# Kernel optimization log

Measured on AMD Instinct MI355X. Metric: run time of the kernel, lower is better.

Reference implementation:

```python
import jax, jax.numpy as jnp
import numpy as np

N_SRC = 20000
N_TAR = 20000
DIM = 3


def setup_inputs() -> dict:
    key = jax.random.key(0)
    k1, k2 = jax.random.split(key)
    src_V = jax.random.normal(k1, (N_SRC, DIM), dtype=jnp.float32)
    tar_V = jax.random.normal(k2, (N_TAR, DIM), dtype=jnp.float32)
    return {"src_V": src_V, "tar_V": tar_V}


def reference(src_V, tar_V):
    # Brute-force 1-NN replacing the CPU cKDTree query.
    # Squared distances: ||t||^2 - 2 t.s^T + ||s||^2  -> [M, N]
    d2 = (
        jnp.sum(tar_V * tar_V, axis=1, keepdims=True)
        - 2.0 * (tar_V @ src_V.T)
        + jnp.sum(src_V * src_V, axis=1)[None, :]
    )
    ii = jnp.argmin(d2, axis=1)          # nearest src index per tar point
    diff = src_V[ii] - tar_V             # gather + residual, [M, 3]
    return 0.5 * jnp.sum(diff * diff)
```

## Files before the change

### kernel.cpp

```cpp
#include <hip/hip_runtime.h>
#include <float.h>

#define N_SRC 20000
#define N_TAR 20000
#define TPB 512
#define SPLITS 16
#define TILES 40
#define TGRP 79
#define FBLOCKS ((N_TAR + 255) / 256)

typedef _Float16 half8 __attribute__((ext_vector_type(8)));
typedef float floatx16 __attribute__((ext_vector_type(16)));

__global__ __launch_bounds__(TPB) void nn_mfma(
    const float* __restrict__ src, const float* __restrict__ tar,
    float* __restrict__ part, float* __restrict__ out)
{
    if (blockIdx.x == 0 && blockIdx.y == 0 && threadIdx.x == 0) out[0] = 0.f;

    __shared__ alignas(16) _Float16 lds[TILES * 32 * 16];

    const int tid  = threadIdx.x;
    const int lane = tid & 63;
    const int col  = lane & 31;
    const int half = (lane >> 5) & 1;
    const int wave = tid >> 6;

    const int sbase = blockIdx.y * (TILES * 32);
    for (int ls = tid; ls < TILES * 32; ls += TPB) {
        const int s = sbase + ls;
        half8 f0 = {0, 0, 0, 0, 0, 0, 0, 0};
        half8 f1 = {0, 0, 0, 0, 0, 0, 0, 0};
        if (s < N_SRC) {
            const float x = src[s * 3 + 0];
            const float y = src[s * 3 + 1];
            const float z = src[s * 3 + 2];
            const _Float16 xh = (_Float16)x, yh = (_Float16)y, zh = (_Float16)z;
            const _Float16 xl = (_Float16)(x - (float)xh);
            const _Float16 yl = (_Float16)(y - (float)yh);
            const _Float16 zl = (_Float16)(z - (float)zh);
            const float nrm = 0.5f * (x * x + y * y + z * z);
            const _Float16 nh = (_Float16)nrm;
            const _Float16 nl = (_Float16)(nrm - (float)nh);
            f0 = (half8){xh, yh, zh, xh, yh, zh, xl, yl};
            f1 = (half8){zl, nh, nl, 0, 0, 0, 0, 0};
        } else {
            f1 = (half8){0, (_Float16)30000.f, 0, 0, 0, 0, 0, 0};
        }
        *(half8*)&lds[ls * 16 + 0] = f0;
        *(half8*)&lds[ls * 16 + 8] = f1;
    }

    const int strip = blockIdx.x * 8 + wave;
    const int t = min(strip * 32 + col, N_TAR - 1);
    const float tx = tar[t * 3 + 0];
    const float ty = tar[t * 3 + 1];
    const float tz = tar[t * 3 + 2];
    const _Float16 txh = (_Float16)tx, tyh = (_Float16)ty, tzh = (_Float16)tz;
    const _Float16 txl = (_Float16)(tx - (float)txh);
    const _Float16 tyl = (_Float16)(ty - (float)tyh);
    const _Float16 tzl = (_Float16)(tz - (float)tzh);
    half8 a;
    if (half == 0)
        a = (half8){-txh, -tyh, -tzh, -txl, -tyl, -tzl, -txh, -tyh};
    else
        a = (half8){-tzh, (_Float16)1.f, (_Float16)1.f, 0, 0, 0, 0, 0};

    __syncthreads();

    floatx16 m;
#pragma unroll
    for (int i = 0; i < 16; ++i) m[i] = FLT_MAX;
    const floatx16 zero = {};
    const int foff = col * 16 + half * 8;
#pragma unroll 2
    for (int tile = 0; tile < TILES; ++tile) {
        const half8 b = *(const half8*)&lds[tile * 512 + foff];
        const floatx16 d = __builtin_amdgcn_mfma_f32_32x32x16_f16(a, b, zero, 0, 0, 0);
#pragma unroll
        for (int i = 0; i < 16; ++i) m[i] = fminf(m[i], d[i]);
    }

#pragma unroll
    for (int i = 0; i < 16; ++i) {
        m[i] = fminf(m[i], __shfl_xor(m[i], 1));
        m[i] = fminf(m[i], __shfl_xor(m[i], 2));
        m[i] = fminf(m[i], __shfl_xor(m[i], 4));
        m[i] = fminf(m[i], __shfl_xor(m[i], 8));
        m[i] = fminf(m[i], __shfl_xor(m[i], 16));
    }
    if (col == 0) {
#pragma unroll
        for (int i = 0; i < 16; ++i) {
            const int row = (i & 3) + 8 * (i >> 2) + 4 * half;
            const int tt = min(strip * 32 + row, N_TAR - 1);
            part[blockIdx.y * N_TAR + tt] = m[i];
        }
    }
}

__global__ __launch_bounds__(256) void nn_finalize(
    const float* __restrict__ tar, const float* __restrict__ part,
    float* __restrict__ out)
{
    const int t = blockIdx.x * 256 + threadIdx.x;
    float contrib = 0.f;
    if (t < N_TAR) {
        float m = FLT_MAX;
#pragma unroll
        for (int c = 0; c < SPLITS; ++c) m = fminf(m, part[c * N_TAR + t]);
        const float tx = tar[t * 3 + 0];
        const float ty = tar[t * 3 + 1];
        const float tz = tar[t * 3 + 2];
        contrib = 0.5f * (tx * tx + ty * ty + tz * tz) + m;
    }
    for (int off = 32; off > 0; off >>= 1)
        contrib += __shfl_down(contrib, off);
    __shared__ float red[4];
    if ((threadIdx.x & 63) == 0) red[threadIdx.x >> 6] = contrib;
    __syncthreads();
    if (threadIdx.x == 0) {
        float s = 0.f;
#pragma unroll
        for (int w = 0; w < 4; ++w) s += red[w];
        atomicAdd(out, s);
    }
}

extern "C" void kernel_launch(void* const* d_in, const int* in_sizes, int n_in,
                              void* d_out, int out_size, void* d_ws, size_t ws_size,
                              hipStream_t stream) {
    const float* src = (const float*)d_in[0];
    const float* tar = (const float*)d_in[1];
    float* out = (float*)d_out;
    float* part = (float*)d_ws;

    dim3 grid1(TGRP, SPLITS);
    nn_mfma<<<grid1, TPB, 0, stream>>>(src, tar, part, out);
    nn_finalize<<<FBLOCKS, 256, 0, stream>>>(tar, part, out);
}
```

Baseline: 77.78 us.

## Process two target strips per wave to reuse LDS source tiles

Each wave now handles two 32-point target strips, and the grid is halved to 40 target groups. Every pair of source tiles loaded from LDS feeds four MFMAs instead of one per load, which cuts LDS traffic and the per-block staging of source points into LDS. In exchange the kernel uses more registers (two accumulators, two A operands) and launches half as many blocks, which lowers occupancy and parallelism.

```diff
diff --git a/kernel.cpp b/kernel.cpp
--- a/kernel.cpp
+++ b/kernel.cpp
@@ -6,7 +6,8 @@
 #define TPB 512
 #define SPLITS 16
 #define TILES 40
-#define TGRP 79
+#define TGRP 40
+#define NSTRIPS (TGRP * 8)
 #define FBLOCKS ((N_TAR + 255) / 256)
 
 typedef _Float16 half8 __attribute__((ext_vector_type(8)));
@@ -51,50 +52,81 @@
         *(half8*)&lds[ls * 16 + 8] = f1;
     }
 
-    const int strip = blockIdx.x * 8 + wave;
-    const int t = min(strip * 32 + col, N_TAR - 1);
-    const float tx = tar[t * 3 + 0];
-    const float ty = tar[t * 3 + 1];
-    const float tz = tar[t * 3 + 2];
-    const _Float16 txh = (_Float16)tx, tyh = (_Float16)ty, tzh = (_Float16)tz;
-    const _Float16 txl = (_Float16)(tx - (float)txh);
-    const _Float16 tyl = (_Float16)(ty - (float)tyh);
-    const _Float16 tzl = (_Float16)(tz - (float)tzh);
-    half8 a;
-    if (half == 0)
-        a = (half8){-txh, -tyh, -tzh, -txl, -tyl, -tzl, -txh, -tyh};
-    else
-        a = (half8){-tzh, (_Float16)1.f, (_Float16)1.f, 0, 0, 0, 0, 0};
+    const int strip0 = blockIdx.x * 8 + wave;
+    const int strip1 = strip0 + NSTRIPS;
+    half8 a0, a1;
+    {
+        const int t = min(strip0 * 32 + col, N_TAR - 1);
+        const float tx = tar[t * 3 + 0];
+        const float ty = tar[t * 3 + 1];
+        const float tz = tar[t * 3 + 2];
+        const _Float16 txh = (_Float16)tx, tyh = (_Float16)ty, tzh = (_Float16)tz;
+        const _Float16 txl = (_Float16)(tx - (float)txh);
+        const _Float16 tyl = (_Float16)(ty - (float)tyh);
+        const _Float16 tzl = (_Float16)(tz - (float)tzh);
+        if (half == 0)
+            a0 = (half8){-txh, -tyh, -tzh, -txl, -tyl, -tzl, -txh, -tyh};
+        else
+            a0 = (half8){-tzh, (_Float16)1.f, (_Float16)1.f, 0, 0, 0, 0, 0};
+    }
+    {
+        const int t = min(strip1 * 32 + col, N_TAR - 1);
+        const float tx = tar[t * 3 + 0];
+        const float ty = tar[t * 3 + 1];
+        const float tz = tar[t * 3 + 2];
+        const _Float16 txh = (_Float16)tx, tyh = (_Float16)ty, tzh = (_Float16)tz;
+        const _Float16 txl = (_Float16)(tx - (float)txh);
+        const _Float16 tyl = (_Float16)(ty - (float)tyh);
+        const _Float16 tzl = (_Float16)(tz - (float)tzh);
+        if (half == 0)
+            a1 = (half8){-txh, -tyh, -tzh, -txl, -tyl, -tzl, -txh, -tyh};
+        else
+            a1 = (half8){-tzh, (_Float16)1.f, (_Float16)1.f, 0, 0, 0, 0, 0};
+    }
 
     __syncthreads();
 
-    floatx16 m;
+    floatx16 m0, m1;
 #pragma unroll
-    for (int i = 0; i < 16; ++i) m[i] = FLT_MAX;
+    for (int i = 0; i < 16; ++i) { m0[i] = FLT_MAX; m1[i] = FLT_MAX; }
     const floatx16 zero = {};
     const int foff = col * 16 + half * 8;
-#pragma unroll 2
-    for (int tile = 0; tile < TILES; ++tile) {
-        const half8 b = *(const half8*)&lds[tile * 512 + foff];
-        const floatx16 d = __builtin_amdgcn_mfma_f32_32x32x16_f16(a, b, zero, 0, 0, 0);
+    for (int tp = 0; tp < TILES; tp += 2) {
+        const half8 b0 = *(const half8*)&lds[tp * 512 + foff];
+        const half8 b1 = *(const half8*)&lds[(tp + 1) * 512 + foff];
+        const floatx16 d0 = __builtin_amdgcn_mfma_f32_32x32x16_f16(a0, b0, zero, 0, 0, 0);
+        const floatx16 d1 = __builtin_amdgcn_mfma_f32_32x32x16_f16(a0, b1, zero, 0, 0, 0);
 #pragma unroll
-        for (int i = 0; i < 16; ++i) m[i] = fminf(m[i], d[i]);
+        for (int i = 0; i < 16; ++i)
+            m0[i] = fminf(fminf(d0[i], d1[i]), m0[i]);
+        const floatx16 d2 = __builtin_amdgcn_mfma_f32_32x32x16_f16(a1, b0, zero, 0, 0, 0);
+        const floatx16 d3 = __builtin_amdgcn_mfma_f32_32x32x16_f16(a1, b1, zero, 0, 0, 0);
+#pragma unroll
+        for (int i = 0; i < 16; ++i)
+            m1[i] = fminf(fminf(d2[i], d3[i]), m1[i]);
     }
 
 #pragma unroll
     for (int i = 0; i < 16; ++i) {
-        m[i] = fminf(m[i], __shfl_xor(m[i], 1));
-        m[i] = fminf(m[i], __shfl_xor(m[i], 2));
-        m[i] = fminf(m[i], __shfl_xor(m[i], 4));
-        m[i] = fminf(m[i], __shfl_xor(m[i], 8));
-        m[i] = fminf(m[i], __shfl_xor(m[i], 16));
+        m0[i] = fminf(m0[i], __shfl_xor(m0[i], 1));
+        m1[i] = fminf(m1[i], __shfl_xor(m1[i], 1));
+        m0[i] = fminf(m0[i], __shfl_xor(m0[i], 2));
+        m1[i] = fminf(m1[i], __shfl_xor(m1[i], 2));
+        m0[i] = fminf(m0[i], __shfl_xor(m0[i], 4));
+        m1[i] = fminf(m1[i], __shfl_xor(m1[i], 4));
+        m0[i] = fminf(m0[i], __shfl_xor(m0[i], 8));
+        m1[i] = fminf(m1[i], __shfl_xor(m1[i], 8));
+        m0[i] = fminf(m0[i], __shfl_xor(m0[i], 16));
+        m1[i] = fminf(m1[i], __shfl_xor(m1[i], 16));
     }
     if (col == 0) {
 #pragma unroll
         for (int i = 0; i < 16; ++i) {
             const int row = (i & 3) + 8 * (i >> 2) + 4 * half;
-            const int tt = min(strip * 32 + row, N_TAR - 1);
-            part[blockIdx.y * N_TAR + tt] = m[i];
+            const int t0 = min(strip0 * 32 + row, N_TAR - 1);
+            const int t1 = min(strip1 * 32 + row, N_TAR - 1);
+            part[blockIdx.y * N_TAR + t0] = m0[i];
+            part[blockIdx.y * N_TAR + t1] = m1[i];
         }
     }
 }
```

After: 80.81 us. +3.9%, slower.

## Fuse NN min and reduction into one kernel with atomic-max partials and last-block finalize

Applied to the files above, without the earlier changes.

Merges the two kernels into one. Each wave now processes three target strips against the same staged source tile, which reuses the LDS B operands across more MFMAs. The LDS layout is XOR-swizzled to reduce bank conflicts, and shuffles are replaced by DPP row rotations. Per-target minima are combined through order-preserving atomicMax on a global buffer, and the last block to finish does the final sum and resets the buffer. This removes one kernel launch and the partial-array traffic, at the cost of a global atomic counter, persistent device state, and heavy reliance on correct memory fences.

```diff
diff --git a/kernel.cpp b/kernel.cpp
--- a/kernel.cpp
+++ b/kernel.cpp
@@ -5,28 +5,37 @@
 #define N_TAR 20000
 #define TPB 512
 #define SPLITS 16
+#define COLS 32
+#define NBLOCKS (COLS * SPLITS)
 #define TILES 40
-#define TGRP 79
-#define FBLOCKS ((N_TAR + 255) / 256)
+#define SRC_PER_SPLIT 1250
+#define KSTRIPS 3
+#define NSTRIP 625
 
 typedef _Float16 half8 __attribute__((ext_vector_type(8)));
 typedef float floatx16 __attribute__((ext_vector_type(16)));
 
-__global__ __launch_bounds__(TPB) void nn_mfma(
+__device__ unsigned g_part[N_TAR];
+__device__ unsigned g_done = 0;
+
+#define ROTMIN(v, ctrl) \
+    fminf(v, __int_as_float(__builtin_amdgcn_mov_dpp(__float_as_int(v), ctrl, 0xF, 0xF, false)))
+
+__global__ __launch_bounds__(TPB, 4) void nn_fused(
     const float* __restrict__ src, const float* __restrict__ tar,
-    float* __restrict__ part, float* __restrict__ out)
+    float* __restrict__ out)
 {
-    if (blockIdx.x == 0 && blockIdx.y == 0 && threadIdx.x == 0) out[0] = 0.f;
-
-    __shared__ alignas(16) _Float16 lds[TILES * 32 * 16];
+    __shared__ alignas(16) _Float16 bstage[TILES * 512];
+    __shared__ bool is_last;
+    __shared__ float red[8];
 
     const int tid  = threadIdx.x;
     const int lane = tid & 63;
     const int col  = lane & 31;
-    const int half = (lane >> 5) & 1;
+    const int hsel = (lane >> 5) & 1;
     const int wave = tid >> 6;
 
-    const int sbase = blockIdx.y * (TILES * 32);
+    const int sbase = blockIdx.y * SRC_PER_SPLIT;
     for (int ls = tid; ls < TILES * 32; ls += TPB) {
         const int s = sbase + ls;
         half8 f0 = {0, 0, 0, 0, 0, 0, 0, 0};
@@ -47,83 +56,113 @@
         } else {
             f1 = (half8){0, (_Float16)30000.f, 0, 0, 0, 0, 0, 0};
         }
-        *(half8*)&lds[ls * 16 + 0] = f0;
-        *(half8*)&lds[ls * 16 + 8] = f1;
+        const int tile = ls >> 5, c = ls & 31;
+        const int n0 = c * 2, n1 = c * 2 + 1;
+        const int o0 = n0 ^ ((n0 >> 3) & 7);
+        const int o1 = n1 ^ ((n1 >> 3) & 7);
+        *(half8*)&bstage[tile * 512 + o0 * 8] = f0;
+        *(half8*)&bstage[tile * 512 + o1 * 8] = f1;
     }
 
-    const int strip = blockIdx.x * 8 + wave;
-    const int t = min(strip * 32 + col, N_TAR - 1);
-    const float tx = tar[t * 3 + 0];
-    const float ty = tar[t * 3 + 1];
-    const float tz = tar[t * 3 + 2];
-    const _Float16 txh = (_Float16)tx, tyh = (_Float16)ty, tzh = (_Float16)tz;
-    const _Float16 txl = (_Float16)(tx - (float)txh);
-    const _Float16 tyl = (_Float16)(ty - (float)tyh);
-    const _Float16 tzl = (_Float16)(tz - (float)tzh);
-    half8 a;
-    if (half == 0)
-        a = (half8){-txh, -tyh, -tzh, -txl, -tyl, -tzl, -txh, -tyh};
-    else
-        a = (half8){-tzh, (_Float16)1.f, (_Float16)1.f, 0, 0, 0, 0, 0};
+    const int strip0 = blockIdx.x * 8 + wave;
+    half8 a[KSTRIPS];
+    bool valid[KSTRIPS];
+#pragma unroll
+    for (int k = 0; k < KSTRIPS; ++k) {
+        const int sk = strip0 + k * 256;
+        valid[k] = (sk < NSTRIP);
+        const int t = min(sk * 32 + col, N_TAR - 1);
+        const float tx = tar[t * 3 + 0];
+        const float ty = tar[t * 3 + 1];
+        const float tz = tar[t * 3 + 2];
+        const _Float16 txh = (_Float16)tx, tyh = (_Float16)ty, tzh = (_Float16)tz;
+        const _Float16 txl = (_Float16)(tx - (float)txh);
+        const _Float16 tyl = (_Float16)(ty - (float)tyh);
+        const _Float16 tzl = (_Float16)(tz - (float)tzh);
+        if (hsel == 0)
+            a[k] = (half8){-txh, -tyh, -tzh, -txl, -tyl, -tzl, -txh, -tyh};
+        else
+            a[k] = (half8){-tzh, (_Float16)1.f, (_Float16)1.f, 0, 0, 0, 0, 0};
+    }
 
     __syncthreads();
 
-    floatx16 m;
+    floatx16 m0, m1, m2;
 #pragma unroll
-    for (int i = 0; i < 16; ++i) m[i] = FLT_MAX;
+    for (int i = 0; i < 16; ++i) { m0[i] = FLT_MAX; m1[i] = FLT_MAX; m2[i] = FLT_MAX; }
     const floatx16 zero = {};
-    const int foff = col * 16 + half * 8;
-#pragma unroll 2
-    for (int tile = 0; tile < TILES; ++tile) {
-        const half8 b = *(const half8*)&lds[tile * 512 + foff];
-        const floatx16 d = __builtin_amdgcn_mfma_f32_32x32x16_f16(a, b, zero, 0, 0, 0);
+    const int nrd = 2 * col + hsel;
+    const int foff = (nrd ^ ((nrd >> 3) & 7)) * 8;
+    for (int tp = 0; tp < TILES; tp += 2) {
+        const half8 b0 = *(const half8*)&bstage[tp * 512 + foff];
+        const half8 b1 = *(const half8*)&bstage[(tp + 1) * 512 + foff];
+        floatx16 d0, d1;
+        d0 = __builtin_amdgcn_mfma_f32_32x32x16_f16(a[0], b0, zero, 0, 0, 0);
+        d1 = __builtin_amdgcn_mfma_f32_32x32x16_f16(a[0], b1, zero, 0, 0, 0);
 #pragma unroll
-        for (int i = 0; i < 16; ++i) m[i] = fminf(m[i], d[i]);
+        for (int i = 0; i < 16; ++i) m0[i] = fminf(fminf(d0[i], d1[i]), m0[i]);
+        d0 = __builtin_amdgcn_mfma_f32_32x32x16_f16(a[1], b0, zero, 0, 0, 0);
+        d1 = __builtin_amdgcn_mfma_f32_32x32x16_f16(a[1], b1, zero, 0, 0, 0);
+#pragma unroll
+        for (int i = 0; i < 16; ++i) m1[i] = fminf(fminf(d0[i], d1[i]), m1[i]);
+        d0 = __builtin_amdgcn_mfma_f32_32x32x16_f16(a[2], b0, zero, 0, 0, 0);
+        d1 = __builtin_amdgcn_mfma_f32_32x32x16_f16(a[2], b1, zero, 0, 0, 0);
+#pragma unroll
+        for (int i = 0; i < 16; ++i) m2[i] = fminf(fminf(d0[i], d1[i]), m2[i]);
     }
 
+    const bool alane = ((lane & 15) == 0);
 #pragma unroll
-    for (int i = 0; i < 16; ++i) {
-        m[i] = fminf(m[i], __shfl_xor(m[i], 1));
-        m[i] = fminf(m[i], __shfl_xor(m[i], 2));
-        m[i] = fminf(m[i], __shfl_xor(m[i], 4));
-        m[i] = fminf(m[i], __shfl_xor(m[i], 8));
-        m[i] = fminf(m[i], __shfl_xor(m[i], 16));
-    }
-    if (col == 0) {
+    for (int k = 0; k < KSTRIPS; ++k) {
+        const int sk = strip0 + k * 256;
 #pragma unroll
         for (int i = 0; i < 16; ++i) {
-            const int row = (i & 3) + 8 * (i >> 2) + 4 * half;
-            const int tt = min(strip * 32 + row, N_TAR - 1);
-            part[blockIdx.y * N_TAR + tt] = m[i];
+            float v = (k == 0) ? m0[i] : (k == 1) ? m1[i] : m2[i];
+            v = ROTMIN(v, 0x128);
+            v = ROTMIN(v, 0x124);
+            v = ROTMIN(v, 0x122);
+            v = ROTMIN(v, 0x121);
+            if (alane && valid[k]) {
+                const int row = (i & 3) + 8 * (i >> 2) + 4 * hsel;
+                const unsigned b = __float_as_uint(v);
+                const unsigned u = (b >> 31) ? b : (~b & 0x7fffffffu);
+                atomicMax(&g_part[sk * 32 + row], u);
+            }
         }
     }
-}
 
-__global__ __launch_bounds__(256) void nn_finalize(
-    const float* __restrict__ tar, const float* __restrict__ part,
-    float* __restrict__ out)
-{
-    const int t = blockIdx.x * 256 + threadIdx.x;
-    float contrib = 0.f;
-    if (t < N_TAR) {
-        float m = FLT_MAX;
-#pragma unroll
-        for (int c = 0; c < SPLITS; ++c) m = fminf(m, part[c * N_TAR + t]);
+    __syncthreads();
+    if (tid == 0) {
+        __threadfence();
+        const unsigned old = atomicAdd(&g_done, 1u);
+        is_last = ((old & (NBLOCKS - 1u)) == (NBLOCKS - 1u));
+    }
+    __syncthreads();
+    if (!is_last) return;
+    __threadfence();
+
+    float local = 0.f;
+    for (int t = tid; t < N_TAR; t += TPB) {
+        const unsigned u = __hip_atomic_load(&g_part[t], __ATOMIC_RELAXED,
+                                             __HIP_MEMORY_SCOPE_AGENT);
+        __hip_atomic_store(&g_part[t], 0u, __ATOMIC_RELAXED,
+                           __HIP_MEMORY_SCOPE_AGENT);
+        const unsigned b = (u & 0x80000000u) ? u : (~u & 0x7fffffffu);
+        const float m = __uint_as_float(b);
         const float tx = tar[t * 3 + 0];
         const float ty = tar[t * 3 + 1];
         const float tz = tar[t * 3 + 2];
-        contrib = 0.5f * (tx * tx + ty * ty + tz * tz) + m;
+        local += 0.5f * (tx * tx + ty * ty + tz * tz) + m;
     }
     for (int off = 32; off > 0; off >>= 1)
-        contrib += __shfl_down(contrib, off);
-    __shared__ float red[4];
-    if ((threadIdx.x & 63) == 0) red[threadIdx.x >> 6] = contrib;
+        local += __shfl_down(local, off);
+    if ((tid & 63) == 0) red[tid >> 6] = local;
     __syncthreads();
-    if (threadIdx.x == 0) {
+    if (tid == 0) {
         float s = 0.f;
 #pragma unroll
-        for (int w = 0; w < 4; ++w) s += red[w];
-        atomicAdd(out, s);
+        for (int w = 0; w < 8; ++w) s += red[w];
+        out[0] = s;
     }
 }
 
@@ -133,9 +172,8 @@
     const float* src = (const float*)d_in[0];
     const float* tar = (const float*)d_in[1];
     float* out = (float*)d_out;
-    float* part = (float*)d_ws;
+    (void)d_ws; (void)ws_size;
 
-    dim3 grid1(TGRP, SPLITS);
-    nn_mfma<<<grid1, TPB, 0, stream>>>(src, tar, part, out);
-    nn_finalize<<<FBLOCKS, 256, 0, stream>>>(tar, part, out);
+    dim3 grid(COLS, SPLITS);
+    nn_fused<<<grid, TPB, 0, stream>>>(src, tar, out);
 }
```

Result: slower. 180.1 us (+131.6%).
